# Kernel optimization log

Hardware: AMD Instinct MI355X
Metric: run time of the kernel (lower is better)

The kernel has to match this reference:

```python
import jax, jax.numpy as jnp
import numpy as np

N, E = 50000, 800000
IN, HID, HEADS, OUT = 128, 32, 8, 40
D1 = HID * HEADS  # 256


def setup_inputs() -> dict:
    key = jax.random.key(0)
    ks = jax.random.split(key, 24)

    def w(k, fin, fout):
        return (jax.random.normal(k, (fin, fout), jnp.float32) / np.sqrt(fin)).astype(jnp.float32)

    def b(k, fout):
        return (jax.random.normal(k, (fout,), jnp.float32) * 0.02).astype(jnp.float32)

    inp = {
        "x": jax.random.normal(ks[0], (N, IN), jnp.float32),
        "edge_index": jax.random.randint(ks[1], (2, E), 0, N, dtype=jnp.int64),
        # layer 1: TransformerConv(IN -> HID, heads=HEADS, concat=True, beta=True)
        "q1w": w(ks[2], IN, D1), "q1b": b(ks[3], D1),
        "k1w": w(ks[4], IN, D1), "k1b": b(ks[5], D1),
        "v1w": w(ks[6], IN, D1), "v1b": b(ks[7], D1),
        "s1w": w(ks[8], IN, D1), "s1b": b(ks[9], D1),
        "b1w": w(ks[10], 3 * D1, 1),
        # layer 2: TransformerConv(D1 -> OUT, heads=1, concat=False, beta=True)
        "q2w": w(ks[11], D1, OUT), "q2b": b(ks[12], OUT),
        "k2w": w(ks[13], D1, OUT), "k2b": b(ks[14], OUT),
        "v2w": w(ks[15], D1, OUT), "v2b": b(ks[16], OUT),
        "s2w": w(ks[17], D1, OUT), "s2b": b(ks[18], OUT),
        "b2w": w(ks[19], 3 * OUT, 1),
    }
    return inp


def _tconv(x, src, dst, qw, qb, kw, kb, vw, vb, sw, sb, bw, heads, ch, concat):
    """PyG TransformerConv (no edge_attr, root_weight=True, beta=True), eval mode."""
    n = x.shape[0]
    q = (x @ qw + qb).reshape(n, heads, ch)
    k = (x @ kw + kb).reshape(n, heads, ch)
    v = (x @ vw + vb).reshape(n, heads, ch)
    # per-edge attention logits: message flows src(j) -> dst(i)
    alpha = jnp.einsum("ehc,ehc->eh", q[dst], k[src]) / np.sqrt(ch)  # [E,H]
    # segment softmax over incoming edges of each dst node
    amax = jax.ops.segment_max(alpha, dst, num_segments=n)  # [N,H]
    a = jnp.exp(alpha - amax[dst])
    asum = jax.ops.segment_sum(a, dst, num_segments=n)  # [N,H]
    attn = a / asum[dst]  # [E,H]
    # scatter-aggregate weighted values
    out = jax.ops.segment_sum(v[src] * attn[:, :, None], dst, num_segments=n)  # [N,H,C]
    out = out.reshape(n, heads * ch) if concat else out.mean(axis=1)
    skip = x @ sw + sb
    beta = jax.nn.sigmoid(jnp.concatenate([out, skip, out - skip], axis=-1) @ bw)  # [N,1]
    return beta * skip + (1.0 - beta) * out


def reference(x, edge_index, q1w, q1b, k1w, k1b, v1w, v1b, s1w, s1b, b1w,
              q2w, q2b, k2w, k2b, v2w, v2b, s2w, s2b, b2w):
    src, dst = edge_index[0], edge_index[1]
    h = jax.nn.elu(_tconv(x, src, dst, q1w, q1b, k1w, k1b, v1w, v1b, s1w, s1b, b1w, HEADS, HID, True))
    return _tconv(h, src, dst, q2w, q2b, k2w, k2b, v2w, v2b, s2w, s2b, b2w, 1, OUT, False)
```

## Files before the change

kernel.cpp:

```cpp
#include <hip/hip_runtime.h>
#include <cstdint>
#include <cstddef>

#define N_NODES 50000
#define N_EDGES 800000
#define IN_F    128
#define HID     32
#define HEADS   8
#define OUT_F   40
#define D1      256
#define W1COLS  1024
#define W2COLS  160
#define CAP     64

#define GFILL_B   3125
#define G1_BX     391
#define G1_BY     8
#define G1_GEMM_B (G1_BX * G1_BY)
#define G1_TOTAL  (GFILL_B + G1_GEMM_B)

typedef unsigned short ushortT;
typedef unsigned char  ucharT;
typedef unsigned short ushortx8 __attribute__((ext_vector_type(8)));
typedef __bf16 bf16x8 __attribute__((ext_vector_type(8)));
typedef float floatx4 __attribute__((ext_vector_type(4)));
typedef float floatx2 __attribute__((ext_vector_type(2)));

__device__ inline ushortT f2bf(float f) {
    union { float f; unsigned int u; } c; c.f = f;
    unsigned int r = c.u + 0x7FFFu + ((c.u >> 16) & 1u);
    return (ushortT)(r >> 16);
}
__device__ inline float bf2f(ushortT h) {
    union { unsigned int u; float f; } c; c.u = ((unsigned int)h) << 16; return c.f;
}

#define PREP_Z_B     196
#define PREP_CONV_B  6250
#define PREP_W1_B    512
#define PREP_W2_B    160
#define PREP_TOTAL_B (PREP_Z_B + PREP_CONV_B + PREP_W1_B + PREP_W2_B)

__global__ __launch_bounds__(256) void k_prep(
        int* __restrict__ cursor,
        const float* __restrict__ x, ushortT* __restrict__ xb,
        const float* __restrict__ q1w, const float* __restrict__ k1w,
        const float* __restrict__ v1w, const float* __restrict__ s1w,
        const float* __restrict__ q1b, const float* __restrict__ k1b,
        const float* __restrict__ v1b, const float* __restrict__ s1b,
        ushortT* __restrict__ W1T, float* __restrict__ b1c,
        const float* __restrict__ q2w, const float* __restrict__ k2w,
        const float* __restrict__ v2w, const float* __restrict__ s2w,
        const float* __restrict__ q2b, const float* __restrict__ k2b,
        const float* __restrict__ v2b, const float* __restrict__ s2b,
        ushortT* __restrict__ W2T, float* __restrict__ b2c) {
    int b = blockIdx.x;
    int tid = threadIdx.x;
    if (b < PREP_Z_B) {
        int i = b * 256 + tid;
        if (i < N_NODES) cursor[i] = 0;
    } else if (b < PREP_Z_B + PREP_CONV_B) {
        int i = (b - PREP_Z_B) * 256 + tid;
        float4 v = reinterpret_cast<const float4*>(x)[i];
        ushort4 o;
        o.x = f2bf(v.x); o.y = f2bf(v.y); o.z = f2bf(v.z); o.w = f2bf(v.w);
        reinterpret_cast<ushort4*>(xb)[i] = o;
    } else if (b < PREP_Z_B + PREP_CONV_B + PREP_W1_B) {
        int t = (b - PREP_Z_B - PREP_CONV_B) * 256 + tid;
        int c = t / IN_F, k = t % IN_F;
        int sel = c >> 8, cc = c & 255;
        const float* w = sel == 0 ? q1w : sel == 1 ? k1w : sel == 2 ? v1w : s1w;
        W1T[(size_t)c * IN_F + k] = f2bf(w[(size_t)k * D1 + cc]);
        if (k == 0) {
            const float* bb = sel == 0 ? q1b : sel == 1 ? k1b : sel == 2 ? v1b : s1b;
            b1c[c] = bb[cc];
        }
    } else {
        int t = (b - PREP_Z_B - PREP_CONV_B - PREP_W1_B) * 256 + tid;
        int c = t / D1, k = t % D1;
        int sel = c / OUT_F, cc = c % OUT_F;
        const float* w = sel == 0 ? q2w : sel == 1 ? k2w : sel == 2 ? v2w : s2w;
        W2T[(size_t)c * D1 + k] = f2bf(w[(size_t)k * OUT_F + cc]);
        if (k == 0) {
            const float* bb = sel == 0 ? q2b : sel == 1 ? k2b : sel == 2 ? v2b : s2b;
            b2c[c] = bb[cc];
        }
    }
}

template<int MODE>
__global__ __launch_bounds__(256) void gemm_mfma_pack(
        const ushortT* __restrict__ A, const ushortT* __restrict__ BT,
        const float* __restrict__ bias, float* __restrict__ QSf,
        ushortT* __restrict__ QSh, ucharT* __restrict__ KV8,
        ushortT* __restrict__ K2V2,
        const int* __restrict__ ei, int* __restrict__ cursor, int* __restrict__ col,
        int M, int K, int Nn) {
    constexpr int TM = 128, TN = 128, TK = 32, LDP = 40;
    __shared__ ushortT smem[TM * LDP + TN * LDP];
    ushortT* As = smem;
    ushortT* Bs = smem + TM * LDP;
    int bx2, by2;
    if (MODE == 1) {
        int t = blockIdx.x;
        int idx;
        bool isFill;
        if (t < 2 * GFILL_B) { isFill = !(t & 1); idx = t >> 1; }
        else                 { isFill = false;    idx = t - GFILL_B; }
        if (isFill) {
            int e = idx * 256 + threadIdx.x;
            if (e < N_EDGES) {
                int dd = ei[N_EDGES + e];
                int p = atomicAdd(&cursor[dd], 1);
                col[dd * CAP + p] = ei[e];
            }
            return;
        }
        bx2 = idx % G1_BX;
        by2 = idx / G1_BX;
    } else {
        bx2 = blockIdx.x;
        by2 = blockIdx.y;
    }
    int tid = threadIdx.x;
    int lane = tid & 63, wave = tid >> 6;
    int bm = bx2 * TM, bn = by2 * TN;
    int wm = (wave & 1) * 64, wn = (wave >> 1) * 64;
    int mrow = lane & 15, g = lane >> 4;
    floatx4 acc[4][4] = {};

    for (int k0 = 0; k0 < K; k0 += TK) {
#pragma unroll
        for (int it = 0; it < 2; ++it) {
            int idx = tid + it * 256;
            int r = idx >> 2, c = (idx & 3) * 8;
            int gm = bm + r;
            ushortx8 val;
            if (gm < M) val = *reinterpret_cast<const ushortx8*>(A + (size_t)gm * K + k0 + c);
            else        val = (ushortx8)0;
            *reinterpret_cast<ushortx8*>(As + r * LDP + c) = val;
        }
#pragma unroll
        for (int it = 0; it < 2; ++it) {
            int idx = tid + it * 256;
            int r = idx >> 2, c = (idx & 3) * 8;
            int gn = bn + r;
            ushortx8 val;
            if (gn < Nn) val = *reinterpret_cast<const ushortx8*>(BT + (size_t)gn * K + k0 + c);
            else         val = (ushortx8)0;
            *reinterpret_cast<ushortx8*>(Bs + r * LDP + c) = val;
        }
        __syncthreads();
        {
            bf16x8 a[4], b[4];
#pragma unroll
            for (int i = 0; i < 4; ++i)
                a[i] = *reinterpret_cast<const bf16x8*>(As + (wm + i * 16 + mrow) * LDP + g * 8);
#pragma unroll
            for (int j = 0; j < 4; ++j)
                b[j] = *reinterpret_cast<const bf16x8*>(Bs + (wn + j * 16 + mrow) * LDP + g * 8);
#pragma unroll
            for (int i = 0; i < 4; ++i)
#pragma unroll
                for (int j = 0; j < 4; ++j)
                    acc[i][j] = __builtin_amdgcn_mfma_f32_16x16x32_bf16(a[i], b[j], acc[i][j], 0, 0, 0);
        }
        __syncthreads();
    }

    if (MODE == 1) {
        float* lds = reinterpret_cast<float*>(smem) + wave * 1088;
        int sec = by2 >> 1;
        int ccbase = (by2 & 1) * 128 + wn;
        int cb4 = (lane & 15) * 4;
        int rlo = lane >> 4;
        float4 bv = *reinterpret_cast<const float4*>(bias + by2 * 128 + wn + cb4);
#pragma unroll
        for (int i = 0; i < 4; ++i) {
#pragma unroll
            for (int j = 0; j < 4; ++j)
#pragma unroll
                for (int r = 0; r < 4; ++r)
                    lds[(g * 4 + r) * 68 + j * 16 + mrow] = acc[i][j][r];
#pragma unroll
            for (int it = 0; it < 4; ++it) {
                int row = it * 4 + rlo;
                int gm = bm + wm + i * 16 + row;
                if (gm >= M) continue;
                float4 v = *reinterpret_cast<float4*>(lds + row * 68 + cb4);
                v.x += bv.x; v.y += bv.y; v.z += bv.z; v.w += bv.w;
                int cc = ccbase + cb4;
                if (sec == 0 || sec == 3) {
                    ushort4 h;
                    h.x = f2bf(v.x); h.y = f2bf(v.y); h.z = f2bf(v.z); h.w = f2bf(v.w);
                    ushortT* dst = QSh + (size_t)gm * 512 + (sec == 3 ? 256 : 0) + cc;
                    *reinterpret_cast<ushort4*>(dst) = h;
                } else {
                    unsigned int pk = 0;
                    pk = __builtin_amdgcn_cvt_pk_fp8_f32(v.x, v.y, pk, false);
                    pk = __builtin_amdgcn_cvt_pk_fp8_f32(v.z, v.w, pk, true);
                    ucharT* dst = KV8 + (size_t)gm * 512 + (sec == 2 ? 256 : 0) + cc;
                    *reinterpret_cast<unsigned int*>(dst) = pk;
                }
            }
        }
    } else {
#pragma unroll
        for (int i = 0; i < 4; ++i) {
#pragma unroll
            for (int j = 0; j < 4; ++j) {
                int gn = bn + wn + j * 16 + mrow;
                if (gn >= Nn) continue;
                float bvs = bias[gn];
#pragma unroll
                for (int r = 0; r < 4; ++r) {
                    int gm = bm + wm + i * 16 + g * 4 + r;
                    if (gm >= M) continue;
                    float val = acc[i][j][r] + bvs;
                    int sec = gn / OUT_F, cc = gn % OUT_F;
                    if (sec == 0)      QSf[(size_t)gm * 80 + cc] = val;
                    else if (sec == 1) K2V2[(size_t)gm * 80 + cc] = f2bf(val);
                    else if (sec == 2) K2V2[(size_t)gm * 80 + 40 + cc] = f2bf(val);
                    else               QSf[(size_t)gm * 80 + 40 + cc] = val;
                }
            }
        }
    }
}

__global__ __launch_bounds__(256) void k_edge1(
        const ushortT* __restrict__ QSh, const ucharT* __restrict__ KV8,
        const float* __restrict__ bw,
        const int* __restrict__ degc, const int* __restrict__ col,
        ushortT* __restrict__ H1b) {
    int gid  = blockIdx.x * blockDim.x + threadIdx.x;
    int node = gid >> 6;
    int lane = threadIdx.x & 63;
    if (node >= N_NODES) return;
    const float scale = 0.17677669529663687f;
    ushort4 qh = *reinterpret_cast<const ushort4*>(QSh + (size_t)node * 512 + lane * 4);
    float4 q;
    q.x = bf2f(qh.x) * scale; q.y = bf2f(qh.y) * scale;
    q.z = bf2f(qh.z) * scale; q.w = bf2f(qh.w) * scale;

    float l = 0.f;
    float4 acc = make_float4(0.f, 0.f, 0.f, 0.f);
    int start = node * CAP;
    int d = degc[node];
    int t = 0;
    for (; t + 2 <= d; t += 2) {
        int j0 = col[start + t];
        int j1 = col[start + t + 1];
        const ucharT* row0 = KV8 + (size_t)j0 * 512 + lane * 4;
        const ucharT* row1 = KV8 + (size_t)j1 * 512 + lane * 4;
        unsigned int ku0 = *reinterpret_cast<const unsigned int*>(row0);
        unsigned int vu0 = *reinterpret_cast<const unsigned int*>(row0 + 256);
        unsigned int ku1 = *reinterpret_cast<const unsigned int*>(row1);
        unsigned int vu1 = *reinterpret_cast<const unsigned int*>(row1 + 256);
        floatx2 k0a = __builtin_amdgcn_cvt_pk_f32_fp8(ku0, false);
        floatx2 k0b = __builtin_amdgcn_cvt_pk_f32_fp8(ku0, true);
        floatx2 k1a = __builtin_amdgcn_cvt_pk_f32_fp8(ku1, false);
        floatx2 k1b = __builtin_amdgcn_cvt_pk_f32_fp8(ku1, true);
        float p0 = q.x * k0a[0] + q.y * k0a[1] + q.z * k0b[0] + q.w * k0b[1];
        float p1 = q.x * k1a[0] + q.y * k1a[1] + q.z * k1b[0] + q.w * k1b[1];
        p0 += __shfl_xor(p0, 1);  p1 += __shfl_xor(p1, 1);
        p0 += __shfl_xor(p0, 2);  p1 += __shfl_xor(p1, 2);
        p0 += __shfl_xor(p0, 4);  p1 += __shfl_xor(p1, 4);
        float e0 = __expf(p0);
        float e1 = __expf(p1);
        l += e0 + e1;
        floatx2 v0a = __builtin_amdgcn_cvt_pk_f32_fp8(vu0, false);
        floatx2 v0b = __builtin_amdgcn_cvt_pk_f32_fp8(vu0, true);
        floatx2 v1a = __builtin_amdgcn_cvt_pk_f32_fp8(vu1, false);
        floatx2 v1b = __builtin_amdgcn_cvt_pk_f32_fp8(vu1, true);
        acc.x += e0 * v0a[0] + e1 * v1a[0];
        acc.y += e0 * v0a[1] + e1 * v1a[1];
        acc.z += e0 * v0b[0] + e1 * v1b[0];
        acc.w += e0 * v0b[1] + e1 * v1b[1];
    }
    if (t < d) {
        int j = col[start + t];
        const ucharT* row = KV8 + (size_t)j * 512 + lane * 4;
        unsigned int ku = *reinterpret_cast<const unsigned int*>(row);
        unsigned int vu = *reinterpret_cast<const unsigned int*>(row + 256);
        floatx2 ka = __builtin_amdgcn_cvt_pk_f32_fp8(ku, false);
        floatx2 kb = __builtin_amdgcn_cvt_pk_f32_fp8(ku, true);
        float p0 = q.x * ka[0] + q.y * ka[1] + q.z * kb[0] + q.w * kb[1];
        p0 += __shfl_xor(p0, 1);
        p0 += __shfl_xor(p0, 2);
        p0 += __shfl_xor(p0, 4);
        float e0 = __expf(p0);
        l += e0;
        floatx2 va = __builtin_amdgcn_cvt_pk_f32_fp8(vu, false);
        floatx2 vb = __builtin_amdgcn_cvt_pk_f32_fp8(vu, true);
        acc.x += e0 * va[0];
        acc.y += e0 * va[1];
        acc.z += e0 * vb[0];
        acc.w += e0 * vb[1];
    }
    float inv = (l > 0.f) ? 1.f / l : 0.f;
    float4 o = make_float4(acc.x * inv, acc.y * inv, acc.z * inv, acc.w * inv);
    ushort4 sh = *reinterpret_cast<const ushort4*>(QSh + (size_t)node * 512 + 256 + lane * 4);
    float4 sk;
    sk.x = bf2f(sh.x); sk.y = bf2f(sh.y); sk.z = bf2f(sh.z); sk.w = bf2f(sh.w);
    const int c4 = lane * 4;
    float4 w0 = *reinterpret_cast<const float4*>(bw + c4);
    float4 w1 = *reinterpret_cast<const float4*>(bw + D1 + c4);
    float4 w2 = *reinterpret_cast<const float4*>(bw + 2 * D1 + c4);
    float part = o.x * w0.x + o.y * w0.y + o.z * w0.z + o.w * w0.w
               + sk.x * w1.x + sk.y * w1.y + sk.z * w1.z + sk.w * w1.w
               + (o.x - sk.x) * w2.x + (o.y - sk.y) * w2.y
               + (o.z - sk.z) * w2.z + (o.w - sk.w) * w2.w;
#pragma unroll
    for (int s = 1; s < 64; s <<= 1) part += __shfl_xor(part, s);
    float beta = 1.f / (1.f + __expf(-part));
    float4 h;
    h.x = beta * sk.x + (1.f - beta) * o.x;
    h.y = beta * sk.y + (1.f - beta) * o.y;
    h.z = beta * sk.z + (1.f - beta) * o.z;
    h.w = beta * sk.w + (1.f - beta) * o.w;
    h.x = h.x > 0.f ? h.x : __expf(h.x) - 1.f;
    h.y = h.y > 0.f ? h.y : __expf(h.y) - 1.f;
    h.z = h.z > 0.f ? h.z : __expf(h.z) - 1.f;
    h.w = h.w > 0.f ? h.w : __expf(h.w) - 1.f;
    ushort4 hb;
    hb.x = f2bf(h.x); hb.y = f2bf(h.y); hb.z = f2bf(h.z); hb.w = f2bf(h.w);
    *reinterpret_cast<ushort4*>(H1b + (size_t)node * D1 + c4) = hb;
}

__global__ __launch_bounds__(256) void k_edge2(
        const float* __restrict__ QS, const ushortT* __restrict__ K2V2,
        const float* __restrict__ bw,
        const int* __restrict__ degc, const int* __restrict__ col,
        float* __restrict__ out) {
    __shared__ float        qbuf[4][40];
    __shared__ float        attn[4][64];
    __shared__ int          jb[4][64];
    __shared__ unsigned int ksm[4][64 * 21];
    int gid  = blockIdx.x * blockDim.x + threadIdx.x;
    int node = gid >> 6;
    int wave = threadIdx.x >> 6;
    int lane = threadIdx.x & 63;
    if (node >= N_NODES) return;
    const float scale = 0.15811388300841897f;
    bool act = lane < OUT_F;
    if (act) qbuf[wave][lane] = QS[(size_t)node * 80 + lane] * scale;

    int d = degc[node];
    if (lane < d) jb[wave][lane] = col[node * CAP + lane];

    const unsigned int* Kdw = reinterpret_cast<const unsigned int*>(K2V2);
    int sr = lane / 20;
    int sc = lane - sr * 20;
    for (int r0 = 0; r0 < d; r0 += 3) {
        int rr = r0 + sr;
        if (lane < 60 && rr < d)
            ksm[wave][rr * 21 + sc] = Kdw[(size_t)jb[wave][rr] * 40 + sc];
    }

    float p = 0.f;
    if (lane < d) {
        float s = 0.f;
#pragma unroll
        for (int c = 0; c < 20; ++c) {
            unsigned int kk = ksm[wave][lane * 21 + c];
            s += qbuf[wave][2 * c]     * bf2f((ushortT)(kk & 0xFFFFu))
               + qbuf[wave][2 * c + 1] * bf2f((ushortT)(kk >> 16));
        }
        p = __expf(s);
    }
    attn[wave][lane] = p;
    float l = p;
#pragma unroll
    for (int s = 1; s < 64; s <<= 1) l += __shfl_xor(l, s);

    float acc = 0.f;
    int ln = act ? lane : 0;
    int e = 0;
    for (; e + 4 <= d; e += 4) {
        int je0 = jb[wave][e],     je1 = jb[wave][e + 1];
        int je2 = jb[wave][e + 2], je3 = jb[wave][e + 3];
        float v0 = bf2f(K2V2[(size_t)je0 * 80 + 40 + ln]);
        float v1 = bf2f(K2V2[(size_t)je1 * 80 + 40 + ln]);
        float v2 = bf2f(K2V2[(size_t)je2 * 80 + 40 + ln]);
        float v3 = bf2f(K2V2[(size_t)je3 * 80 + 40 + ln]);
        acc += (attn[wave][e] * v0 + attn[wave][e + 1] * v1)
             + (attn[wave][e + 2] * v2 + attn[wave][e + 3] * v3);
    }
    for (; e < d; ++e)
        acc += attn[wave][e] * bf2f(K2V2[(size_t)jb[wave][e] * 80 + 40 + ln]);

    float inv = (l > 0.f) ? 1.f / l : 0.f;
    float o  = acc * inv;
    float sk = act ? QS[(size_t)node * 80 + 40 + lane] : 0.f;
    float part = act ? (o * bw[lane] + sk * bw[OUT_F + lane] + (o - sk) * bw[2 * OUT_F + lane]) : 0.f;
#pragma unroll
    for (int s = 1; s < 64; s <<= 1) part += __shfl_xor(part, s);
    float beta = 1.f / (1.f + __expf(-part));
    if (act) out[(size_t)node * OUT_F + lane] = beta * sk + (1.f - beta) * o;
}

extern "C" void kernel_launch(void* const* d_in, const int* in_sizes, int n_in,
                              void* d_out, int out_size, void* d_ws, size_t ws_size,
                              hipStream_t stream) {
    const float* x   = (const float*)d_in[0];
    const int*   ei  = (const int*)d_in[1];
    const float* q1w = (const float*)d_in[2];
    const float* q1b = (const float*)d_in[3];
    const float* k1w = (const float*)d_in[4];
    const float* k1b = (const float*)d_in[5];
    const float* v1w = (const float*)d_in[6];
    const float* v1b = (const float*)d_in[7];
    const float* s1w = (const float*)d_in[8];
    const float* s1b = (const float*)d_in[9];
    const float* b1w = (const float*)d_in[10];
    const float* q2w = (const float*)d_in[11];
    const float* q2b = (const float*)d_in[12];
    const float* k2w = (const float*)d_in[13];
    const float* k2b = (const float*)d_in[14];
    const float* v2w = (const float*)d_in[15];
    const float* v2b = (const float*)d_in[16];
    const float* s2w = (const float*)d_in[17];
    const float* s2b = (const float*)d_in[18];
    const float* b2w = (const float*)d_in[19];
    float* out = (float*)d_out;

    char* w = (char*)d_ws;
    ushortT* QSh = (ushortT*)w;
    ucharT*  KV8 = (ucharT*)(w + 51200000);
    ushortT* H1b = (ushortT*)(w + 102400000);
    ushortT* xb  = (ushortT*)(w + 128000000);
    ushortT* W1T = (ushortT*)(w + 140800000);
    ushortT* W2T = (ushortT*)(w + 141062144);
    float*   b1c = (float*)(w + 141144064);
    float*   b2c = (float*)(w + 141148160);
    int* cursor  = (int*)(w + 141149184);
    int* col     = cursor + N_NODES;
    float*   QS2  = (float*)w;
    ushortT* K2V2 = (ushortT*)(w + 51200000);

    k_prep<<<PREP_TOTAL_B, 256, 0, stream>>>(
        cursor, x, xb,
        q1w, k1w, v1w, s1w, q1b, k1b, v1b, s1b, W1T, b1c,
        q2w, k2w, v2w, s2w, q2b, k2b, v2b, s2b, W2T, b2c);

    gemm_mfma_pack<1><<<G1_TOTAL, 256, 0, stream>>>(
        xb, W1T, b1c, nullptr, QSh, KV8, nullptr,
        ei, cursor, col, N_NODES, IN_F, W1COLS);

    k_edge1<<<(N_NODES * 64) / 256, 256, 0, stream>>>(QSh, KV8, b1w, cursor, col, H1b);

    dim3 g2((N_NODES + 127) / 128, (W2COLS + 127) / 128);
    gemm_mfma_pack<2><<<g2, 256, 0, stream>>>(H1b, W2T, b2c, QS2, nullptr, nullptr,
                                              K2V2, nullptr, nullptr, nullptr,
                                              N_NODES, D1, W2COLS);

    k_edge2<<<(N_NODES * 64) / 256, 256, 0, stream>>>(QS2, K2V2, b2w, cursor, col, out);
}
```

Baseline: 362.3 us.

## Interleave K/V fp8 rows and unroll edge1 gather by four with DPP reductions

The layer-1 GEMM epilogue now writes K and V fp8 values interleaved per channel group, so each lane fetches its K and V bytes with a single 8-byte load instead of two 4-byte loads. The edge1 loop is unrolled to four neighbours, loads the column indices as an int4, uses packed float2 math, and replaces the shuffle-based 8-lane reduction with DPP row operations. The cursor zeroing moves from the prep kernel to a hipMemsetAsync, and the node index is made wave-uniform. The int4 index load relies on CAP alignment, and the extra memset adds a separate launch.

```diff
diff --git a/kernel.cpp b/kernel.cpp
--- a/kernel.cpp
+++ b/kernel.cpp
@@ -21,6 +21,7 @@
 
 typedef unsigned short ushortT;
 typedef unsigned char  ucharT;
+typedef unsigned long long ullT;
 typedef unsigned short ushortx8 __attribute__((ext_vector_type(8)));
 typedef __bf16 bf16x8 __attribute__((ext_vector_type(8)));
 typedef float floatx4 __attribute__((ext_vector_type(4)));
@@ -35,14 +36,23 @@
     union { unsigned int u; float f; } c; c.u = ((unsigned int)h) << 16; return c.f;
 }
 
-#define PREP_Z_B     196
+__device__ inline float red8(float x) {
+    int v;
+    v = __builtin_amdgcn_update_dpp(0, __float_as_int(x), 0xB1, 0xF, 0xF, false);
+    x += __int_as_float(v);
+    v = __builtin_amdgcn_update_dpp(0, __float_as_int(x), 0x4E, 0xF, 0xF, false);
+    x += __int_as_float(v);
+    v = __builtin_amdgcn_update_dpp(0, __float_as_int(x), 0x141, 0xF, 0xF, false);
+    x += __int_as_float(v);
+    return x;
+}
+
 #define PREP_CONV_B  6250
 #define PREP_W1_B    512
 #define PREP_W2_B    160
-#define PREP_TOTAL_B (PREP_Z_B + PREP_CONV_B + PREP_W1_B + PREP_W2_B)
+#define PREP_TOTAL_B (PREP_CONV_B + PREP_W1_B + PREP_W2_B)
 
 __global__ __launch_bounds__(256) void k_prep(
-        int* __restrict__ cursor,
         const float* __restrict__ x, ushortT* __restrict__ xb,
         const float* __restrict__ q1w, const float* __restrict__ k1w,
         const float* __restrict__ v1w, const float* __restrict__ s1w,
@@ -56,17 +66,14 @@
         ushortT* __restrict__ W2T, float* __restrict__ b2c) {
     int b = blockIdx.x;
     int tid = threadIdx.x;
-    if (b < PREP_Z_B) {
+    if (b < PREP_CONV_B) {
         int i = b * 256 + tid;
-        if (i < N_NODES) cursor[i] = 0;
-    } else if (b < PREP_Z_B + PREP_CONV_B) {
-        int i = (b - PREP_Z_B) * 256 + tid;
         float4 v = reinterpret_cast<const float4*>(x)[i];
         ushort4 o;
         o.x = f2bf(v.x); o.y = f2bf(v.y); o.z = f2bf(v.z); o.w = f2bf(v.w);
         reinterpret_cast<ushort4*>(xb)[i] = o;
-    } else if (b < PREP_Z_B + PREP_CONV_B + PREP_W1_B) {
-        int t = (b - PREP_Z_B - PREP_CONV_B) * 256 + tid;
+    } else if (b < PREP_CONV_B + PREP_W1_B) {
+        int t = (b - PREP_CONV_B) * 256 + tid;
         int c = t / IN_F, k = t % IN_F;
         int sel = c >> 8, cc = c & 255;
         const float* w = sel == 0 ? q1w : sel == 1 ? k1w : sel == 2 ? v1w : s1w;
@@ -76,7 +83,7 @@
             b1c[c] = bb[cc];
         }
     } else {
-        int t = (b - PREP_Z_B - PREP_CONV_B - PREP_W1_B) * 256 + tid;
+        int t = (b - PREP_CONV_B - PREP_W1_B) * 256 + tid;
         int c = t / D1, k = t % D1;
         int sel = c / OUT_F, cc = c % OUT_F;
         const float* w = sel == 0 ? q2w : sel == 1 ? k2w : sel == 2 ? v2w : s2w;
@@ -199,7 +206,7 @@
                     unsigned int pk = 0;
                     pk = __builtin_amdgcn_cvt_pk_fp8_f32(v.x, v.y, pk, false);
                     pk = __builtin_amdgcn_cvt_pk_fp8_f32(v.z, v.w, pk, true);
-                    ucharT* dst = KV8 + (size_t)gm * 512 + (sec == 2 ? 256 : 0) + cc;
+                    ucharT* dst = KV8 + (size_t)gm * 512 + cc * 2 + (sec == 2 ? 4 : 0);
                     *reinterpret_cast<unsigned int*>(dst) = pk;
                 }
             }
@@ -234,72 +241,82 @@
         const int* __restrict__ degc, const int* __restrict__ col,
         ushortT* __restrict__ H1b) {
     int gid  = blockIdx.x * blockDim.x + threadIdx.x;
-    int node = gid >> 6;
     int lane = threadIdx.x & 63;
+    int node = __builtin_amdgcn_readfirstlane(gid >> 6);
     if (node >= N_NODES) return;
     const float scale = 0.17677669529663687f;
     ushort4 qh = *reinterpret_cast<const ushort4*>(QSh + (size_t)node * 512 + lane * 4);
-    float4 q;
-    q.x = bf2f(qh.x) * scale; q.y = bf2f(qh.y) * scale;
-    q.z = bf2f(qh.z) * scale; q.w = bf2f(qh.w) * scale;
+    floatx2 q01, q23;
+    q01[0] = bf2f(qh.x) * scale; q01[1] = bf2f(qh.y) * scale;
+    q23[0] = bf2f(qh.z) * scale; q23[1] = bf2f(qh.w) * scale;
 
     float l = 0.f;
-    float4 acc = make_float4(0.f, 0.f, 0.f, 0.f);
-    int start = node * CAP;
+    floatx2 acc01 = {0.f, 0.f}, acc23 = {0.f, 0.f};
+    const int* colp = col + node * CAP;
     int d = degc[node];
+    int voff = lane * 8;
     int t = 0;
-    for (; t + 2 <= d; t += 2) {
-        int j0 = col[start + t];
-        int j1 = col[start + t + 1];
-        const ucharT* row0 = KV8 + (size_t)j0 * 512 + lane * 4;
-        const ucharT* row1 = KV8 + (size_t)j1 * 512 + lane * 4;
-        unsigned int ku0 = *reinterpret_cast<const unsigned int*>(row0);
-        unsigned int vu0 = *reinterpret_cast<const unsigned int*>(row0 + 256);
-        unsigned int ku1 = *reinterpret_cast<const unsigned int*>(row1);
-        unsigned int vu1 = *reinterpret_cast<const unsigned int*>(row1 + 256);
-        floatx2 k0a = __builtin_amdgcn_cvt_pk_f32_fp8(ku0, false);
-        floatx2 k0b = __builtin_amdgcn_cvt_pk_f32_fp8(ku0, true);
-        floatx2 k1a = __builtin_amdgcn_cvt_pk_f32_fp8(ku1, false);
-        floatx2 k1b = __builtin_amdgcn_cvt_pk_f32_fp8(ku1, true);
-        float p0 = q.x * k0a[0] + q.y * k0a[1] + q.z * k0b[0] + q.w * k0b[1];
-        float p1 = q.x * k1a[0] + q.y * k1a[1] + q.z * k1b[0] + q.w * k1b[1];
-        p0 += __shfl_xor(p0, 1);  p1 += __shfl_xor(p1, 1);
-        p0 += __shfl_xor(p0, 2);  p1 += __shfl_xor(p1, 2);
-        p0 += __shfl_xor(p0, 4);  p1 += __shfl_xor(p1, 4);
+    for (; t + 4 <= d; t += 4) {
+        int4 js = *reinterpret_cast<const int4*>(colp + t);
+        const ucharT* r0 = KV8 + ((size_t)js.x << 9);
+        const ucharT* r1 = KV8 + ((size_t)js.y << 9);
+        const ucharT* r2 = KV8 + ((size_t)js.z << 9);
+        const ucharT* r3 = KV8 + ((size_t)js.w << 9);
+        ullT kv0 = *reinterpret_cast<const ullT*>(r0 + voff);
+        ullT kv1 = *reinterpret_cast<const ullT*>(r1 + voff);
+        ullT kv2 = *reinterpret_cast<const ullT*>(r2 + voff);
+        ullT kv3 = *reinterpret_cast<const ullT*>(r3 + voff);
+        floatx2 k0a = __builtin_amdgcn_cvt_pk_f32_fp8((unsigned)kv0, false);
+        floatx2 k0b = __builtin_amdgcn_cvt_pk_f32_fp8((unsigned)kv0, true);
+        floatx2 k1a = __builtin_amdgcn_cvt_pk_f32_fp8((unsigned)kv1, false);
+        floatx2 k1b = __builtin_amdgcn_cvt_pk_f32_fp8((unsigned)kv1, true);
+        floatx2 k2a = __builtin_amdgcn_cvt_pk_f32_fp8((unsigned)kv2, false);
+        floatx2 k2b = __builtin_amdgcn_cvt_pk_f32_fp8((unsigned)kv2, true);
+        floatx2 k3a = __builtin_amdgcn_cvt_pk_f32_fp8((unsigned)kv3, false);
+        floatx2 k3b = __builtin_amdgcn_cvt_pk_f32_fp8((unsigned)kv3, true);
+        floatx2 pd0 = q01 * k0a + q23 * k0b;
+        floatx2 pd1 = q01 * k1a + q23 * k1b;
+        floatx2 pd2 = q01 * k2a + q23 * k2b;
+        floatx2 pd3 = q01 * k3a + q23 * k3b;
+        float p0 = red8(pd0[0] + pd0[1]);
+        float p1 = red8(pd1[0] + pd1[1]);
+        float p2 = red8(pd2[0] + pd2[1]);
+        float p3 = red8(pd3[0] + pd3[1]);
         float e0 = __expf(p0);
         float e1 = __expf(p1);
-        l += e0 + e1;
-        floatx2 v0a = __builtin_amdgcn_cvt_pk_f32_fp8(vu0, false);
-        floatx2 v0b = __builtin_amdgcn_cvt_pk_f32_fp8(vu0, true);
-        floatx2 v1a = __builtin_amdgcn_cvt_pk_f32_fp8(vu1, false);
-        floatx2 v1b = __builtin_amdgcn_cvt_pk_f32_fp8(vu1, true);
-        acc.x += e0 * v0a[0] + e1 * v1a[0];
-        acc.y += e0 * v0a[1] + e1 * v1a[1];
-        acc.z += e0 * v0b[0] + e1 * v1b[0];
-        acc.w += e0 * v0b[1] + e1 * v1b[1];
-    }
-    if (t < d) {
-        int j = col[start + t];
-        const ucharT* row = KV8 + (size_t)j * 512 + lane * 4;
-        unsigned int ku = *reinterpret_cast<const unsigned int*>(row);
-        unsigned int vu = *reinterpret_cast<const unsigned int*>(row + 256);
-        floatx2 ka = __builtin_amdgcn_cvt_pk_f32_fp8(ku, false);
-        floatx2 kb = __builtin_amdgcn_cvt_pk_f32_fp8(ku, true);
-        float p0 = q.x * ka[0] + q.y * ka[1] + q.z * kb[0] + q.w * kb[1];
-        p0 += __shfl_xor(p0, 1);
-        p0 += __shfl_xor(p0, 2);
-        p0 += __shfl_xor(p0, 4);
-        float e0 = __expf(p0);
-        l += e0;
-        floatx2 va = __builtin_amdgcn_cvt_pk_f32_fp8(vu, false);
-        floatx2 vb = __builtin_amdgcn_cvt_pk_f32_fp8(vu, true);
-        acc.x += e0 * va[0];
-        acc.y += e0 * va[1];
-        acc.z += e0 * vb[0];
-        acc.w += e0 * vb[1];
+        float e2 = __expf(p2);
+        float e3 = __expf(p3);
+        l += (e0 + e1) + (e2 + e3);
+        floatx2 v0a = __builtin_amdgcn_cvt_pk_f32_fp8((unsigned)(kv0 >> 32), false);
+        floatx2 v0b = __builtin_amdgcn_cvt_pk_f32_fp8((unsigned)(kv0 >> 32), true);
+        floatx2 v1a = __builtin_amdgcn_cvt_pk_f32_fp8((unsigned)(kv1 >> 32), false);
+        floatx2 v1b = __builtin_amdgcn_cvt_pk_f32_fp8((unsigned)(kv1 >> 32), true);
+        floatx2 v2a = __builtin_amdgcn_cvt_pk_f32_fp8((unsigned)(kv2 >> 32), false);
+        floatx2 v2b = __builtin_amdgcn_cvt_pk_f32_fp8((unsigned)(kv2 >> 32), true);
+        floatx2 v3a = __builtin_amdgcn_cvt_pk_f32_fp8((unsigned)(kv3 >> 32), false);
+        floatx2 v3b = __builtin_amdgcn_cvt_pk_f32_fp8((unsigned)(kv3 >> 32), true);
+        floatx2 e0v = {e0, e0}, e1v = {e1, e1}, e2v = {e2, e2}, e3v = {e3, e3};
+        acc01 += e0v * v0a; acc23 += e0v * v0b;
+        acc01 += e1v * v1a; acc23 += e1v * v1b;
+        acc01 += e2v * v2a; acc23 += e2v * v2b;
+        acc01 += e3v * v3a; acc23 += e3v * v3b;
+    }
+    for (; t < d; ++t) {
+        int j = colp[t];
+        ullT kv = *reinterpret_cast<const ullT*>(KV8 + ((size_t)j << 9) + voff);
+        floatx2 ka = __builtin_amdgcn_cvt_pk_f32_fp8((unsigned)kv, false);
+        floatx2 kb = __builtin_amdgcn_cvt_pk_f32_fp8((unsigned)kv, true);
+        floatx2 pd = q01 * ka + q23 * kb;
+        float p = red8(pd[0] + pd[1]);
+        float e = __expf(p);
+        l += e;
+        floatx2 va = __builtin_amdgcn_cvt_pk_f32_fp8((unsigned)(kv >> 32), false);
+        floatx2 vb = __builtin_amdgcn_cvt_pk_f32_fp8((unsigned)(kv >> 32), true);
+        floatx2 ev = {e, e};
+        acc01 += ev * va; acc23 += ev * vb;
     }
     float inv = (l > 0.f) ? 1.f / l : 0.f;
-    float4 o = make_float4(acc.x * inv, acc.y * inv, acc.z * inv, acc.w * inv);
+    float4 o = make_float4(acc01[0] * inv, acc01[1] * inv, acc23[0] * inv, acc23[1] * inv);
     ushort4 sh = *reinterpret_cast<const ushort4*>(QSh + (size_t)node * 512 + 256 + lane * 4);
     float4 sk;
     sk.x = bf2f(sh.x); sk.y = bf2f(sh.y); sk.z = bf2f(sh.z); sk.w = bf2f(sh.w);
@@ -439,8 +456,10 @@
     float*   QS2  = (float*)w;
     ushortT* K2V2 = (ushortT*)(w + 51200000);
 
+    hipMemsetAsync(cursor, 0, N_NODES * sizeof(int), stream);
+
     k_prep<<<PREP_TOTAL_B, 256, 0, stream>>>(
-        cursor, x, xb,
+        x, xb,
         q1w, k1w, v1w, s1w, q1b, k1b, v1b, s1b, W1T, b1c,
         q2w, k2w, v2w, s2w, q2b, k2b, v2b, s2b, W2T, b2c);
 
```

Measured after the change: 350.5 us. 1.03x faster.
